# Kernel tuning notes

Measured on AMD Instinct MI355X. Metric: run time of the kernel, lower is better.

Reference implementation:

```python
import jax, jax.numpy as jnp
import numpy as np

N_HEADS = 16
NEG = -1000000000.0  # masked_fill value from the original code


def setup_inputs() -> dict:
    key = jax.random.key(0)
    ks = jax.random.split(key, 7)
    D = 1024
    x = jax.random.normal(ks[0], (2, 2048, D), dtype=jnp.float32)
    s = 1.0 / np.sqrt(D)
    Wq = jax.random.normal(ks[1], (D, D), dtype=jnp.float32) * s
    bq = jax.random.normal(ks[2], (D,), dtype=jnp.float32) * 0.01
    Wk = jax.random.normal(ks[3], (D, D), dtype=jnp.float32) * s
    bk = jax.random.normal(ks[4], (D,), dtype=jnp.float32) * 0.01
    Wv = jax.random.normal(ks[5], (D, D), dtype=jnp.float32) * s
    bv = jax.random.normal(ks[6], (D,), dtype=jnp.float32) * 0.01
    return {"x": x, "Wq": Wq, "bq": bq, "Wk": Wk, "bk": bk, "Wv": Wv, "bv": bv}


def reference(x, Wq, bq, Wk, bk, Wv, bv):
    B, S, D = x.shape
    H = N_HEADS
    dh = D // H
    # nn.Linear: x @ W.T + b
    Q = (x @ Wq.T + bq).reshape(B, S, H, dh)
    K = (x @ Wk.T + bk).reshape(B, S, H, dh)
    V = (x @ Wv.T + bv).reshape(B, S, H, dh)
    # NOTE: original scales by sqrt(n_heads), not sqrt(d_head) -- faithful.
    scale = jnp.asarray(H, x.dtype) ** 0.5
    scores = jnp.einsum('bqhd,bkhd->bhqk', Q, K) / scale  # [B,H,S,S]
    # Original: mask = triu(ones, diag=1); scores.masked_fill(mask == 0, -1e9)
    # i.e. positions where the STRICT-UPPER mask is False (lower triangle incl.
    # diagonal) get -1e9. Faithful reproduction of that (buggy) behavior.
    triu = jnp.triu(jnp.ones((S, S), dtype=bool), k=1)  # [S,S]
    scores = jnp.where(triu[None, None, :, :], scores, jnp.asarray(NEG, x.dtype))
    probs = jax.nn.softmax(scores, axis=-1)
    # dropout is identity at inference
    out = jnp.einsum('bhqk,bkhd->bqhd', probs, V).reshape(B, S, D)
    return out
```

## Files before the change

kernel.cpp:

```cpp
#include <hip/hip_runtime.h>
#include <stdint.h>

typedef unsigned short u16;
typedef __attribute__((ext_vector_type(8))) short bf16x8;
typedef __attribute__((ext_vector_type(4))) float floatx4;

#define MFMA16(a, b, c) __builtin_amdgcn_mfma_f32_16x16x32_bf16(a, b, c, 0, 0, 0)

#if __has_builtin(__builtin_amdgcn_exp2f)
#define EXP2(x) __builtin_amdgcn_exp2f(x)
#else
#define EXP2(x) __expf(0.6931471805599453f * (x))
#endif

__device__ __forceinline__ u16 f2bf(float f) {
  unsigned u = __builtin_bit_cast(unsigned, f);
  return (u16)((u + 0x7FFFu + ((u >> 16) & 1u)) >> 16);
}
__device__ __forceinline__ unsigned pkbf(float a, float b) {
  unsigned ua = __builtin_bit_cast(unsigned, a);
  unsigned ub = __builtin_bit_cast(unsigned, b);
  return ((ua + 0x8000u) >> 16) | ((ub + 0x8000u) & 0xFFFF0000u);
}
__device__ __forceinline__ float bf2f(u16 v) {
  return __builtin_bit_cast(float, (unsigned)v << 16);
}

__device__ __forceinline__ void glds16(void* lds, const void* g) {
  __builtin_amdgcn_global_load_lds((const __attribute__((address_space(1))) void*)g,
                                   (__attribute__((address_space(3))) void*)lds,
                                   16, 0, 0);
}

__global__ __launch_bounds__(256) void cvt_all(
    const float* __restrict__ x, const float* __restrict__ w0,
    const float* __restrict__ w1, const float* __restrict__ w2,
    u16* __restrict__ xb, u16* __restrict__ Wb) {
  const int bid = blockIdx.x;
  const float* src;
  u16* dst;
  int i;
  if (bid < 4096) {
    src = x; dst = xb; i = bid * 256 + threadIdx.x;
  } else {
    const int z = (bid - 4096) >> 10;
    src = (z == 0) ? w0 : (z == 1) ? w1 : w2;
    dst = Wb + (size_t)z * (1024 * 1024);
    i = ((bid - 4096) & 1023) * 256 + threadIdx.x;
  }
  float4 f = reinterpret_cast<const float4*>(src)[i];
  ushort4 o;
  o.x = f2bf(f.x); o.y = f2bf(f.y); o.z = f2bf(f.z); o.w = f2bf(f.w);
  reinterpret_cast<ushort4*>(dst)[i] = o;
}

__global__ __launch_bounds__(256, 2) void qkv_gemm(
    const u16* __restrict__ xb, const u16* __restrict__ Wb,
    const float* __restrict__ bq, const float* __restrict__ bk,
    const float* __restrict__ bv,
    u16* __restrict__ Qb, u16* __restrict__ Kb, u16* __restrict__ VTb) {
  __shared__ __attribute__((aligned(16))) u16 As[256 * 64];
  __shared__ __attribute__((aligned(16))) u16 Bs[128 * 64];

  const int tid = threadIdx.x;
  const int w = tid >> 6, lane = tid & 63;
  const int lo = lane & 15, quad = lane >> 4;
  const int which = blockIdx.z;
  const int m0 = blockIdx.x * 256, n0 = blockIdx.y * 128;

  const u16* W = Wb + (size_t)which * (1024 * 1024);

  floatx4 acc[4][8];
  for (int i = 0; i < 4; ++i)
    for (int j = 0; j < 8; ++j) acc[i][j] = (floatx4)0.f;

  const int arow = lane >> 3;
  const int aswz = ((lane & 7) ^ arow) * 8;

  for (int kt = 0; kt < 16; ++kt) {
    const int k0 = kt * 64;
    for (int j = 0; j < 8; ++j) {
      const int seg = w * 8 + j;
      glds16(As + seg * 512, xb + (size_t)(m0 + seg * 8 + arow) * 1024 + k0 + aswz);
    }
    for (int j = 0; j < 4; ++j) {
      const int seg = w * 4 + j;
      glds16(Bs + seg * 512, W + (size_t)(n0 + seg * 8 + arow) * 1024 + k0 + aswz);
    }
    __syncthreads();
    for (int kk = 0; kk < 2; ++kk) {
      const int swz = ((kk * 4 + quad) ^ (lo & 7)) * 8;
      bf16x8 af[4], bfr[8];
      for (int mt = 0; mt < 4; ++mt)
        af[mt] = *reinterpret_cast<const bf16x8*>(As + (w * 64 + mt * 16 + lo) * 64 + swz);
      for (int nt = 0; nt < 8; ++nt)
        bfr[nt] = *reinterpret_cast<const bf16x8*>(Bs + (nt * 16 + lo) * 64 + swz);
      for (int mt = 0; mt < 4; ++mt)
        for (int nt = 0; nt < 8; ++nt)
          acc[mt][nt] = MFMA16(af[mt], bfr[nt], acc[mt][nt]);
    }
    __syncthreads();
  }

  const float* bias = (which == 0) ? bq : (which == 1) ? bk : bv;
  float bb[8];
  for (int nt = 0; nt < 8; ++nt) bb[nt] = bias[n0 + nt * 16 + lo];
  const int b = m0 >> 11;
  const int ms = (m0 & 2047) + w * 64;

  if (which < 2) {
    const float scl = (which == 0) ? 0.36067376022224085f : 1.0f;
    u16* Tw = As + w * (16 * 72);
    for (int half = 0; half < 2; ++half) {
      const int hblk = (n0 >> 6) + half;
      u16* dst = ((which == 0) ? Qb : Kb) +
                 ((size_t)(b * 16 + hblk) * 2048 + ms) * 64;
      for (int it = 0; it < 4; ++it) {
        for (int jt = 0; jt < 4; ++jt) {
          const int nt = half * 4 + jt;
          for (int r = 0; r < 4; ++r) {
            const int m = quad * 4 + r, col = jt * 16 + lo;
            Tw[m * 72 + (((col >> 3) ^ (m & 7)) * 8) + (col & 7)] =
                f2bf((acc[it][nt][r] + bb[nt]) * scl);
          }
        }
        for (int rd = 0; rd < 2; ++rd) {
          const int sr = rd * 8 + (lane >> 3), d8 = lane & 7;
          bf16x8 v = *reinterpret_cast<const bf16x8*>(Tw + sr * 72 + ((d8 ^ (sr & 7)) * 8));
          *reinterpret_cast<bf16x8*>(dst + (size_t)(it * 16 + sr) * 64 + d8 * 8) = v;
        }
      }
    }
  } else {
    for (int c = 0; c < 4; ++c) {
      if (w == c) {
        for (int mt = 0; mt < 4; ++mt)
          for (int nt = 0; nt < 8; ++nt)
            for (int r = 0; r < 4; ++r) {
              const int n = nt * 16 + lo;
              const int m = mt * 16 + quad * 4 + r;
              As[n * 72 + (((m >> 3) ^ (n & 7)) * 8) + (m & 7)] =
                  f2bf(acc[mt][nt][r] + bb[nt]);
            }
      }
      __syncthreads();
      for (int rd = 0; rd < 4; ++rd) {
        const int n = (tid >> 3) + rd * 32, m8 = tid & 7;
        bf16x8 v = *reinterpret_cast<const bf16x8*>(As + n * 72 + ((m8 ^ (n & 7)) * 8));
        const int ng = n0 + n, h = ng >> 6, d = ng & 63;
        const int s = (m0 & 2047) + c * 64 + m8 * 8;
        *reinterpret_cast<bf16x8*>(VTb + ((size_t)(b * 16 + h) * 64 + d) * 2048 + s) = v;
      }
      __syncthreads();
    }
  }
}

__global__ __launch_bounds__(256, 2) void attn(
    const u16* __restrict__ Qb, const u16* __restrict__ Kb,
    const u16* __restrict__ VTb, float* __restrict__ out) {
  __shared__ __attribute__((aligned(16))) u16 Ks[2][64 * 64];
  __shared__ __attribute__((aligned(16))) u16 Vs[2][64 * 64];
  __shared__ __attribute__((aligned(16))) u16 Pt[4][2][16 * 64];

  const int L = blockIdx.x;
  const int bh = L & 31;
  const int s5 = L >> 5;
  const int qs = (s5 < 8) ? s5 : 23 - s5;
  const int kstart = 2 * qs;

  const int tid = threadIdx.x, w = tid >> 6, lane = tid & 63;
  const int lo = lane & 15, quad = lane >> 4;

  const u16* Qh = Qb + (size_t)bh * (2048 * 64);
  const u16* Kh = Kb + (size_t)bh * (2048 * 64);
  const u16* Vh = VTb + (size_t)bh * (64 * 2048);

  int qrow[2];
  bf16x8 qf[2][2];
  for (int s = 0; s < 2; ++s) {
    qrow[s] = qs * 128 + w * 32 + s * 16 + lo;
    qf[s][0] = *reinterpret_cast<const bf16x8*>(Qh + (size_t)qrow[s] * 64 + quad * 8);
    qf[s][1] = *reinterpret_cast<const bf16x8*>(Qh + (size_t)qrow[s] * 64 + 32 + quad * 8);
  }

  float lrun[2] = {0.f, 0.f};
  floatx4 acc[2][4];
  for (int s = 0; s < 2; ++s)
    for (int dt = 0; dt < 4; ++dt) acc[s][dt] = (floatx4)0.f;

  const int srow8 = lane >> 3, sblk = lane & 7;
  const int sswz = (sblk ^ srow8) * 8;

  for (int j = 0; j < 2; ++j) {
    const int b8 = (w * 2 + j) * 8;
    glds16(&Ks[0][b8 * 64], Kh + (size_t)(kstart * 64 + b8 + srow8) * 64 + sswz);
    glds16(&Vs[0][b8 * 64], Vh + (size_t)(b8 + srow8) * 2048 + kstart * 64 + sswz);
  }
  __syncthreads();

  for (int kt = kstart; kt < 32; ++kt) {
    const int cur = (kt - kstart) & 1, nxt = cur ^ 1;
    if (kt < 31)
      for (int j = 0; j < 2; ++j) {
        const int b8 = (w * 2 + j) * 8;
        glds16(&Ks[nxt][b8 * 64], Kh + (size_t)((kt + 1) * 64 + b8 + srow8) * 64 + sswz);
        glds16(&Vs[nxt][b8 * 64], Vh + (size_t)(b8 + srow8) * 2048 + (kt + 1) * 64 + sswz);
      }
    const u16* ksb = Ks[cur];
    const u16* vsb = Vs[cur];

    const int d2 = kt - 2 * qs;
    const bool skip = (d2 == 0) && (w >= 2);
    const bool maskp = ((d2 == 0) && (w < 2)) || ((d2 == 1) && (w >= 2));

    if (!skip) {
      floatx4 sc[2][4];
      for (int s = 0; s < 2; ++s)
        for (int t = 0; t < 4; ++t) sc[s][t] = (floatx4)0.f;
      for (int kk = 0; kk < 2; ++kk) {
        const int swz = ((kk * 4 + quad) ^ (lo & 7)) * 8;
        for (int t = 0; t < 4; ++t) {
          bf16x8 ka = *reinterpret_cast<const bf16x8*>(ksb + (t * 16 + lo) * 64 + swz);
          sc[0][t] = MFMA16(ka, qf[0][kk], sc[0][t]);
          sc[1][t] = MFMA16(ka, qf[1][kk], sc[1][t]);
        }
      }

      for (int s = 0; s < 2; ++s) {
        u16* ptw = &Pt[w][s][0];
        for (int t = 0; t < 4; ++t) {
          float p0 = EXP2(sc[s][t][0]), p1 = EXP2(sc[s][t][1]);
          float p2 = EXP2(sc[s][t][2]), p3 = EXP2(sc[s][t][3]);
          if (maskp) {
            const int key = kt * 64 + t * 16 + quad * 4;
            p0 = (key + 0 > qrow[s]) ? p0 : 0.f;
            p1 = (key + 1 > qrow[s]) ? p1 : 0.f;
            p2 = (key + 2 > qrow[s]) ? p2 : 0.f;
            p3 = (key + 3 > qrow[s]) ? p3 : 0.f;
          }
          lrun[s] += (p0 + p1) + (p2 + p3);
          u16* pdst = ptw + lo * 64 +
                      (((2 * t + (quad >> 1)) ^ (lo & 7)) * 8) + (quad & 1) * 4;
          *reinterpret_cast<uint2*>(pdst) = make_uint2(pkbf(p0, p1), pkbf(p2, p3));
        }
      }

      for (int kk = 0; kk < 2; ++kk) {
        const int swz = ((kk * 4 + quad) ^ (lo & 7)) * 8;
        bf16x8 pb0 = *reinterpret_cast<const bf16x8*>(&Pt[w][0][lo * 64] + swz);
        bf16x8 pb1 = *reinterpret_cast<const bf16x8*>(&Pt[w][1][lo * 64] + swz);
        for (int dt = 0; dt < 4; ++dt) {
          bf16x8 va = *reinterpret_cast<const bf16x8*>(vsb + (dt * 16 + lo) * 64 + swz);
          acc[0][dt] = MFMA16(va, pb0, acc[0][dt]);
          acc[1][dt] = MFMA16(va, pb1, acc[1][dt]);
        }
      }
    }
    __syncthreads();
  }

  const int b = bh >> 4, h = bh & 15;
  for (int s = 0; s < 2; ++s) {
    float l = lrun[s];
    l += __shfl_xor(l, 16);
    l += __shfl_xor(l, 32);
    if (l != 0.f) {
      const float rl = 1.f / l;
      float* op = out + ((size_t)(b * 2048 + qrow[s])) * 1024 + h * 64 + quad * 4;
      for (int dt = 0; dt < 4; ++dt) {
        float4 o4;
        o4.x = acc[s][dt][0] * rl; o4.y = acc[s][dt][1] * rl;
        o4.z = acc[s][dt][2] * rl; o4.w = acc[s][dt][3] * rl;
        *reinterpret_cast<float4*>(op + dt * 16) = o4;
      }
    }
  }
}

__global__ __launch_bounds__(256) void fix2047(const u16* __restrict__ VTb,
                                               float* __restrict__ out) {
  const int bh = blockIdx.x;
  const u16* Vh = VTb + (size_t)bh * (64 * 2048);
  const int t = threadIdx.x;
  const int d = t >> 2, j = t & 3;
  float s = 0.f;
  const u16* row = Vh + (size_t)d * 2048 + j * 512;
  for (int i = 0; i < 64; ++i) {
    bf16x8 v = *reinterpret_cast<const bf16x8*>(row + i * 8);
    for (int e = 0; e < 8; ++e) s += bf2f((u16)v[e]);
  }
  s += __shfl_xor(s, 1);
  s += __shfl_xor(s, 2);
  if (j == 0) {
    const int b = bh >> 4, h = bh & 15;
    out[((size_t)(b * 2048 + 2047)) * 1024 + h * 64 + d] = s * (1.f / 2048.f);
  }
}

extern "C" void kernel_launch(void* const* d_in, const int* in_sizes, int n_in,
                              void* d_out, int out_size, void* d_ws, size_t ws_size,
                              hipStream_t stream) {
  const float* x  = (const float*)d_in[0];
  const float* Wq = (const float*)d_in[1];
  const float* bq = (const float*)d_in[2];
  const float* Wk = (const float*)d_in[3];
  const float* bk = (const float*)d_in[4];
  const float* Wv = (const float*)d_in[5];
  const float* bv = (const float*)d_in[6];
  float* out = (float*)d_out;

  char* ws = (char*)d_ws;
  u16* xb  = (u16*)(ws);
  u16* Wb  = (u16*)(ws + (8u << 20));
  u16* Qb  = (u16*)(ws + (14u << 20));
  u16* Kb  = (u16*)(ws + (22u << 20));
  u16* VTb = (u16*)(ws + (30u << 20));

  cvt_all<<<7168, 256, 0, stream>>>(x, Wq, Wk, Wv, xb, Wb);
  qkv_gemm<<<dim3(16, 8, 3), 256, 0, stream>>>(xb, Wb, bq, bk, bv, Qb, Kb, VTb);
  attn<<<dim3(512), 256, 0, stream>>>(Qb, Kb, VTb, out);
  fix2047<<<dim3(32), 256, 0, stream>>>(VTb, out);
}
```

Before: 162.6 us.

## Shrink QKV GEMM tile to 128x128 with 2x2 warp grid and raise occupancy

The QKV projection GEMM now uses 128x128 output tiles instead of 256x128. The four warps are arranged 2x2, each owning a 64x64 sub-tile, and the grid doubles to 768 blocks. Less LDS and fewer accumulators per block allow three blocks per CU (launch bounds raised to 3 for both GEMM and attention). The epilogues are adapted to the new layout, P packing in attention switches to per-element ushort4 rounding, and compiler memory barriers are added. The trade-off is lower data reuse per tile, and higher occupancy bounds may force register spills.

```diff
diff --git a/kernel.cpp b/kernel.cpp
--- a/kernel.cpp
+++ b/kernel.cpp
@@ -6,6 +6,7 @@
 typedef __attribute__((ext_vector_type(4))) float floatx4;
 
 #define MFMA16(a, b, c) __builtin_amdgcn_mfma_f32_16x16x32_bf16(a, b, c, 0, 0, 0)
+#define MEMFENCE asm volatile("" ::: "memory")
 
 #if __has_builtin(__builtin_amdgcn_exp2f)
 #define EXP2(x) __builtin_amdgcn_exp2f(x)
@@ -17,10 +18,8 @@
   unsigned u = __builtin_bit_cast(unsigned, f);
   return (u16)((u + 0x7FFFu + ((u >> 16) & 1u)) >> 16);
 }
-__device__ __forceinline__ unsigned pkbf(float a, float b) {
-  unsigned ua = __builtin_bit_cast(unsigned, a);
-  unsigned ub = __builtin_bit_cast(unsigned, b);
-  return ((ua + 0x8000u) >> 16) | ((ub + 0x8000u) & 0xFFFF0000u);
+__device__ __forceinline__ u16 f2bf_hu(float f) {
+  return (u16)((__builtin_bit_cast(unsigned, f) + 0x8000u) >> 16);
 }
 __device__ __forceinline__ float bf2f(u16 v) {
   return __builtin_bit_cast(float, (unsigned)v << 16);
@@ -54,101 +53,97 @@
   reinterpret_cast<ushort4*>(dst)[i] = o;
 }
 
-__global__ __launch_bounds__(256, 2) void qkv_gemm(
+__global__ __launch_bounds__(256, 3) void qkv_gemm(
     const u16* __restrict__ xb, const u16* __restrict__ Wb,
     const float* __restrict__ bq, const float* __restrict__ bk,
     const float* __restrict__ bv,
     u16* __restrict__ Qb, u16* __restrict__ Kb, u16* __restrict__ VTb) {
-  __shared__ __attribute__((aligned(16))) u16 As[256 * 64];
-  __shared__ __attribute__((aligned(16))) u16 Bs[128 * 64];
+  __shared__ __attribute__((aligned(16))) u16 smem[2 * 128 * 64];
+  u16* As = smem;
+  u16* Bs = smem + 128 * 64;
 
   const int tid = threadIdx.x;
   const int w = tid >> 6, lane = tid & 63;
   const int lo = lane & 15, quad = lane >> 4;
   const int which = blockIdx.z;
-  const int m0 = blockIdx.x * 256, n0 = blockIdx.y * 128;
+  const int m0 = blockIdx.x * 128, n0 = blockIdx.y * 128;
 
   const u16* W = Wb + (size_t)which * (1024 * 1024);
-
-  floatx4 acc[4][8];
+  const int wm = (w >> 1) * 64, wn = (w & 1) * 64;
+
+  floatx4 acc[4][4];
   for (int i = 0; i < 4; ++i)
-    for (int j = 0; j < 8; ++j) acc[i][j] = (floatx4)0.f;
+    for (int j = 0; j < 4; ++j) acc[i][j] = (floatx4)0.f;
 
   const int arow = lane >> 3;
   const int aswz = ((lane & 7) ^ arow) * 8;
 
   for (int kt = 0; kt < 16; ++kt) {
     const int k0 = kt * 64;
-    for (int j = 0; j < 8; ++j) {
-      const int seg = w * 8 + j;
-      glds16(As + seg * 512, xb + (size_t)(m0 + seg * 8 + arow) * 1024 + k0 + aswz);
-    }
     for (int j = 0; j < 4; ++j) {
       const int seg = w * 4 + j;
+      glds16(As + seg * 512, xb + (size_t)(m0 + seg * 8 + arow) * 1024 + k0 + aswz);
       glds16(Bs + seg * 512, W + (size_t)(n0 + seg * 8 + arow) * 1024 + k0 + aswz);
     }
     __syncthreads();
     for (int kk = 0; kk < 2; ++kk) {
       const int swz = ((kk * 4 + quad) ^ (lo & 7)) * 8;
-      bf16x8 af[4], bfr[8];
-      for (int mt = 0; mt < 4; ++mt)
-        af[mt] = *reinterpret_cast<const bf16x8*>(As + (w * 64 + mt * 16 + lo) * 64 + swz);
-      for (int nt = 0; nt < 8; ++nt)
-        bfr[nt] = *reinterpret_cast<const bf16x8*>(Bs + (nt * 16 + lo) * 64 + swz);
-      for (int mt = 0; mt < 4; ++mt)
-        for (int nt = 0; nt < 8; ++nt)
-          acc[mt][nt] = MFMA16(af[mt], bfr[nt], acc[mt][nt]);
+      bf16x8 af[4], bfr[4];
+      for (int it = 0; it < 4; ++it)
+        af[it] = *reinterpret_cast<const bf16x8*>(As + (wm + it * 16 + lo) * 64 + swz);
+      for (int jt = 0; jt < 4; ++jt)
+        bfr[jt] = *reinterpret_cast<const bf16x8*>(Bs + (wn + jt * 16 + lo) * 64 + swz);
+      for (int it = 0; it < 4; ++it)
+        for (int jt = 0; jt < 4; ++jt)
+          acc[it][jt] = MFMA16(af[it], bfr[jt], acc[it][jt]);
     }
     __syncthreads();
   }
 
   const float* bias = (which == 0) ? bq : (which == 1) ? bk : bv;
-  float bb[8];
-  for (int nt = 0; nt < 8; ++nt) bb[nt] = bias[n0 + nt * 16 + lo];
+  float bb[4];
+  for (int jt = 0; jt < 4; ++jt) bb[jt] = bias[n0 + wn + jt * 16 + lo];
   const int b = m0 >> 11;
-  const int ms = (m0 & 2047) + w * 64;
 
   if (which < 2) {
     const float scl = (which == 0) ? 0.36067376022224085f : 1.0f;
-    u16* Tw = As + w * (16 * 72);
-    for (int half = 0; half < 2; ++half) {
-      const int hblk = (n0 >> 6) + half;
-      u16* dst = ((which == 0) ? Qb : Kb) +
-                 ((size_t)(b * 16 + hblk) * 2048 + ms) * 64;
-      for (int it = 0; it < 4; ++it) {
-        for (int jt = 0; jt < 4; ++jt) {
-          const int nt = half * 4 + jt;
-          for (int r = 0; r < 4; ++r) {
-            const int m = quad * 4 + r, col = jt * 16 + lo;
-            Tw[m * 72 + (((col >> 3) ^ (m & 7)) * 8) + (col & 7)] =
-                f2bf((acc[it][nt][r] + bb[nt]) * scl);
-          }
+    u16* Tw = smem + w * (16 * 72);
+    const int hblk = (n0 + wn) >> 6;
+    u16* dst = ((which == 0) ? Qb : Kb) +
+               ((size_t)(b * 16 + hblk) * 2048 + ((m0 & 2047) + wm)) * 64;
+    for (int it = 0; it < 4; ++it) {
+      for (int jt = 0; jt < 4; ++jt)
+        for (int r = 0; r < 4; ++r) {
+          const int m = quad * 4 + r, col = jt * 16 + lo;
+          Tw[m * 72 + (((col >> 3) ^ (m & 7)) * 8) + (col & 7)] =
+              f2bf((acc[it][jt][r] + bb[jt]) * scl);
         }
-        for (int rd = 0; rd < 2; ++rd) {
-          const int sr = rd * 8 + (lane >> 3), d8 = lane & 7;
-          bf16x8 v = *reinterpret_cast<const bf16x8*>(Tw + sr * 72 + ((d8 ^ (sr & 7)) * 8));
-          *reinterpret_cast<bf16x8*>(dst + (size_t)(it * 16 + sr) * 64 + d8 * 8) = v;
-        }
-      }
+      MEMFENCE;
+      for (int rd = 0; rd < 2; ++rd) {
+        const int sr = rd * 8 + (lane >> 3), d8 = lane & 7;
+        bf16x8 v = *reinterpret_cast<const bf16x8*>(Tw + sr * 72 + ((d8 ^ (sr & 7)) * 8));
+        *reinterpret_cast<bf16x8*>(dst + (size_t)(it * 16 + sr) * 64 + d8 * 8) = v;
+      }
+      MEMFENCE;
     }
   } else {
-    for (int c = 0; c < 4; ++c) {
-      if (w == c) {
-        for (int mt = 0; mt < 4; ++mt)
-          for (int nt = 0; nt < 8; ++nt)
+    for (int pass = 0; pass < 2; ++pass) {
+      if ((wm >> 6) == pass) {
+        for (int it = 0; it < 4; ++it)
+          for (int jt = 0; jt < 4; ++jt)
             for (int r = 0; r < 4; ++r) {
-              const int n = nt * 16 + lo;
-              const int m = mt * 16 + quad * 4 + r;
-              As[n * 72 + (((m >> 3) ^ (n & 7)) * 8) + (m & 7)] =
-                  f2bf(acc[mt][nt][r] + bb[nt]);
+              const int n = wn + jt * 16 + lo;
+              const int m = it * 16 + quad * 4 + r;
+              smem[n * 72 + (((m >> 3) ^ (n & 7)) * 8) + (m & 7)] =
+                  f2bf(acc[it][jt][r] + bb[jt]);
             }
       }
       __syncthreads();
       for (int rd = 0; rd < 4; ++rd) {
         const int n = (tid >> 3) + rd * 32, m8 = tid & 7;
-        bf16x8 v = *reinterpret_cast<const bf16x8*>(As + n * 72 + ((m8 ^ (n & 7)) * 8));
+        bf16x8 v = *reinterpret_cast<const bf16x8*>(smem + n * 72 + ((m8 ^ (n & 7)) * 8));
         const int ng = n0 + n, h = ng >> 6, d = ng & 63;
-        const int s = (m0 & 2047) + c * 64 + m8 * 8;
+        const int s = (m0 & 2047) + pass * 64 + m8 * 8;
         *reinterpret_cast<bf16x8*>(VTb + ((size_t)(b * 16 + h) * 64 + d) * 2048 + s) = v;
       }
       __syncthreads();
@@ -156,7 +151,7 @@
   }
 }
 
-__global__ __launch_bounds__(256, 2) void attn(
+__global__ __launch_bounds__(256, 3) void attn(
     const u16* __restrict__ Qb, const u16* __restrict__ Kb,
     const u16* __restrict__ VTb, float* __restrict__ out) {
   __shared__ __attribute__((aligned(16))) u16 Ks[2][64 * 64];
@@ -240,34 +235,40 @@
             p3 = (key + 3 > qrow[s]) ? p3 : 0.f;
           }
           lrun[s] += (p0 + p1) + (p2 + p3);
+          ushort4 pk;
+          pk.x = f2bf_hu(p0); pk.y = f2bf_hu(p1);
+          pk.z = f2bf_hu(p2); pk.w = f2bf_hu(p3);
           u16* pdst = ptw + lo * 64 +
                       (((2 * t + (quad >> 1)) ^ (lo & 7)) * 8) + (quad & 1) * 4;
-          *reinterpret_cast<uint2*>(pdst) = make_uint2(pkbf(p0, p1), pkbf(p2, p3));
+          *reinterpret_cast<ushort4*>(pdst) = pk;
         }
       }
+      MEMFENCE;
 
       for (int kk = 0; kk < 2; ++kk) {
-        const int swz = ((kk * 4 + quad) ^ (lo & 7)) * 8;
-        bf16x8 pb0 = *reinterpret_cast<const bf16x8*>(&Pt[w][0][lo * 64] + swz);
-        bf16x8 pb1 = *reinterpret_cast<const bf16x8*>(&Pt[w][1][lo * 64] + swz);
+        const int pswz = ((kk * 4 + quad) ^ (lo & 7)) * 8;
+        bf16x8 pb0 = *reinterpret_cast<const bf16x8*>(&Pt[w][0][lo * 64] + pswz);
+        bf16x8 pb1 = *reinterpret_cast<const bf16x8*>(&Pt[w][1][lo * 64] + pswz);
         for (int dt = 0; dt < 4; ++dt) {
-          bf16x8 va = *reinterpret_cast<const bf16x8*>(vsb + (dt * 16 + lo) * 64 + swz);
+          bf16x8 va = *reinterpret_cast<const bf16x8*>(
+              vsb + (dt * 16 + lo) * 64 + pswz);
           acc[0][dt] = MFMA16(va, pb0, acc[0][dt]);
           acc[1][dt] = MFMA16(va, pb1, acc[1][dt]);
         }
       }
+      MEMFENCE;
     }
     __syncthreads();
   }
 
-  const int b = bh >> 4, h = bh & 15;
+  const int b = bh >> 4, hh = bh & 15;
   for (int s = 0; s < 2; ++s) {
     float l = lrun[s];
     l += __shfl_xor(l, 16);
     l += __shfl_xor(l, 32);
     if (l != 0.f) {
       const float rl = 1.f / l;
-      float* op = out + ((size_t)(b * 2048 + qrow[s])) * 1024 + h * 64 + quad * 4;
+      float* op = out + ((size_t)(b * 2048 + qrow[s])) * 1024 + hh * 64 + quad * 4;
       for (int dt = 0; dt < 4; ++dt) {
         float4 o4;
         o4.x = acc[s][dt][0] * rl; o4.y = acc[s][dt][1] * rl;
@@ -318,7 +319,7 @@
   u16* VTb = (u16*)(ws + (30u << 20));
 
   cvt_all<<<7168, 256, 0, stream>>>(x, Wq, Wk, Wv, xb, Wb);
-  qkv_gemm<<<dim3(16, 8, 3), 256, 0, stream>>>(xb, Wb, bq, bk, bv, Qb, Kb, VTb);
+  qkv_gemm<<<dim3(32, 8, 3), 256, 0, stream>>>(xb, Wb, bq, bk, bv, Qb, Kb, VTb);
   attn<<<dim3(512), 256, 0, stream>>>(Qb, Kb, VTb, out);
   fix2047<<<dim3(32), 256, 0, stream>>>(VTb, out);
 }
```

Result: faster. 158.9 us (-2.3%).
